# Performance work log

Hardware: AMD Instinct MI355X
Metric: run time of the kernel (lower is better)

Reference implementation:

```python
import jax, jax.numpy as jnp
import numpy as np

B, K, D, H, T, S = 8192, 32, 768, 256, 16, 2  # batch, candidates, d_model, hidden, topics, shots
MAX_SHOT = 8
TEMP = 0.1


def _l2n(x, eps=1e-12):
    return x / jnp.clip(jnp.linalg.norm(x, axis=-1, keepdims=True), eps)


def setup_inputs() -> dict:
    key = jax.random.key(0)
    ks = jax.random.split(key, 20)
    f32 = jnp.float32
    rn = lambda k, shape, s: jax.random.normal(k, shape, f32) * s
    inp = {}
    inp['query_emb'] = jax.random.normal(ks[0], (B, D), f32)
    inp['cand_emb'] = jax.random.normal(ks[1], (B, K, D), f32)
    inp['W_in'] = rn(ks[2], (H, D), 0.03)              # input_proj (bias=False)
    inp['Wq_a'] = rn(ks[3], (H, H), 0.05)              # MHA in-proj q
    inp['Wk_a'] = rn(ks[4], (H, H), 0.05)
    inp['Wv_a'] = rn(ks[5], (H, H), 0.05)
    inp['bq_a'] = jnp.zeros((H,), f32)
    inp['bk_a'] = jnp.zeros((H,), f32)
    inp['bv_a'] = jnp.zeros((H,), f32)
    inp['Wo_a'] = rn(ks[6], (H, H), 0.05)              # MHA out-proj
    inp['bo_a'] = jnp.zeros((H,), f32)
    inp['ln_w'] = jnp.ones((H,), f32)
    inp['ln_b'] = jnp.zeros((H,), f32)
    inp['Wq'] = jnp.eye(H, dtype=f32) + rn(ks[7], (H, H), 0.01)   # query_proj (eye init + noise)
    inp['Wc'] = jnp.eye(H, dtype=f32) + rn(ks[8], (H, H), 0.01)   # cand_proj
    inp['W_ih'] = rn(ks[9], (3 * H, H), 0.05)          # GRUCell ih (r,z,n)
    inp['W_hh'] = rn(ks[10], (3 * H, H), 0.05)
    inp['b_ih'] = jnp.zeros((3 * H,), f32)
    inp['b_hh'] = jnp.zeros((3 * H,), f32)
    inp['step_emb'] = rn(ks[11], (MAX_SHOT, H), 0.02)
    inp['topic_protos'] = rn(ks[12], (T, H), 0.02)
    inp['Wqt'] = rn(ks[13], (T, H), 0.05)              # query_topic_head
    inp['bqt'] = jnp.zeros((T,), f32)
    inp['cover_lambda'] = jnp.array(-2.0, f32)
    return inp


def reference(query_emb, cand_emb, W_in, Wq_a, Wk_a, Wv_a, bq_a, bk_a, bv_a,
              Wo_a, bo_a, ln_w, ln_b, Wq, Wc, W_ih, W_hh, b_ih, b_hh,
              step_emb, topic_protos, Wqt, bqt, cover_lambda):
    Bd = query_emb.shape[0]
    # input projection 768 -> 256
    qr = query_emb @ W_in.T                                # [B,H]
    cr = jnp.einsum('bkd,hd->bkh', cand_emb, W_in)         # [B,K,H]
    # single-head cross-attention (query len 1, eval mode -> no dropout)
    q = qr @ Wq_a.T + bq_a
    k = jnp.einsum('bkh,gh->bkg', cr, Wk_a) + bk_a
    v = jnp.einsum('bkh,gh->bkg', cr, Wv_a) + bv_a
    attn = jax.nn.softmax(jnp.einsum('bh,bkh->bk', q, k) / jnp.sqrt(jnp.float32(H)))
    ctx = jnp.einsum('bk,bkh->bh', attn, v) @ Wo_a.T + bo_a
    # residual + LayerNorm
    x = ctx + qr
    mu = jnp.mean(x, -1, keepdims=True)
    var = jnp.var(x, -1, keepdims=True)
    qe = (x - mu) / jnp.sqrt(var + 1e-5) * ln_w + ln_b
    # pointer projections + L2 normalize
    h = _l2n(qe @ Wq.T)                                    # [B,H]
    cn = _l2n(jnp.einsum('bkh,gh->bkg', cr, Wc))           # [B,K,H]
    topic_probs = jax.nn.softmax(jnp.einsum('bkh,th->bkt', cn, _l2n(topic_protos)))  # [B,K,T]
    need = jax.nn.softmax(h @ Wqt.T + bqt)                 # [B,T]
    lam = jax.nn.softplus(cover_lambda)
    sel = jnp.zeros((Bd, K), bool)
    covered = jnp.zeros((Bd, T), jnp.float32)
    rows = jnp.arange(Bd)
    logits, preds = [], []
    for step in range(S):
        h_step = _l2n(h + step_emb[min(step, MAX_SHOT - 1)])
        scores = jnp.einsum('bh,bkh->bk', h_step, cn) / TEMP
        if step > 0:
            uncov = jnp.clip(1.0 - covered, 0.0, 1.0)
            gain = jnp.einsum('bt,bkt->bk', need * uncov, topic_probs)
            scores = scores + lam * gain
        scores = jnp.where(sel, -100.0, scores)
        logits.append(scores)
        idx = jnp.argmax(scores, axis=-1)                  # labels=None -> greedy feedback
        preds.append(idx)
        sel = sel.at[rows, idx].set(True)
        chosen = cn[rows, idx]                             # [B,H]
        covered = jnp.minimum(covered + topic_probs[rows, idx], 1.0)
        # GRUCell update
        gi = chosen @ W_ih.T + b_ih
        gh = h @ W_hh.T + b_hh
        ir, iz, ig = jnp.split(gi, 3, axis=-1)
        hr, hz, hg = jnp.split(gh, 3, axis=-1)
        r = jax.nn.sigmoid(ir + hr)
        z = jax.nn.sigmoid(iz + hz)
        n = jnp.tanh(ig + r * hg)
        h = _l2n((1.0 - z) * n + z * h)
    return jnp.stack(logits, 1), jnp.stack(preds, 1)       # [B,S,K], [B,S]
```

## Files before the change

kernel.cpp:

```cpp
#include <hip/hip_runtime.h>
#include <math.h>

#define B_ 8192
#define K_ 32
#define D_ 768
#define H_ 256
#define T_ 16
#define S_ 2

typedef unsigned int uint;
typedef unsigned short ushort;
typedef __attribute__((ext_vector_type(8))) short bf16x8;
typedef __attribute__((ext_vector_type(4))) float f32x4;

__device__ __forceinline__ float wsum(float v) {
  v += __shfl_xor(v, 32); v += __shfl_xor(v, 16); v += __shfl_xor(v, 8);
  v += __shfl_xor(v, 4);  v += __shfl_xor(v, 2);  v += __shfl_xor(v, 1);
  return v;
}
__device__ __forceinline__ float wmaxr(float v) {
  v = fmaxf(v, __shfl_xor(v, 32)); v = fmaxf(v, __shfl_xor(v, 16));
  v = fmaxf(v, __shfl_xor(v, 8));  v = fmaxf(v, __shfl_xor(v, 4));
  v = fmaxf(v, __shfl_xor(v, 2));  v = fmaxf(v, __shfl_xor(v, 1));
  return v;
}

__device__ __forceinline__ void split4(const float4 f, uint2& h, uint2& lo) {
  const uint ux = __float_as_uint(f.x), uy = __float_as_uint(f.y);
  const uint uz = __float_as_uint(f.z), uw = __float_as_uint(f.w);
  h.x = (uy & 0xFFFF0000u) | (ux >> 16);
  h.y = (uw & 0xFFFF0000u) | (uz >> 16);
  const float rx = f.x - __uint_as_float(ux & 0xFFFF0000u);
  const float ry = f.y - __uint_as_float(uy & 0xFFFF0000u);
  const float rz = f.z - __uint_as_float(uz & 0xFFFF0000u);
  const float rw = f.w - __uint_as_float(uw & 0xFFFF0000u);
  lo.x = (__float_as_uint(ry) & 0xFFFF0000u) | (__float_as_uint(rx) >> 16);
  lo.y = (__float_as_uint(rw) & 0xFFFF0000u) | (__float_as_uint(rz) >> 16);
}

__device__ __forceinline__ float dot4(const float4 a, const float4 b) {
  float s = a.x * b.x;
  s = fmaf(a.y, b.y, s); s = fmaf(a.z, b.z, s); s = fmaf(a.w, b.w, s);
  return s;
}


__global__ __launch_bounds__(256)
void fold_kernel(const float* __restrict__ Wk_a, const float* __restrict__ Wv_a,
                 const float* __restrict__ Wc,  const float* __restrict__ W_in,
                 float* __restrict__ WkinT, float* __restrict__ Wv_in,
                 ushort* __restrict__ Bh, ushort* __restrict__ Bl)
{
  const int i = blockIdx.x;
  const int m = blockIdx.y;
  const float* Wx = (m == 0) ? Wk_a : ((m == 1) ? Wv_a : Wc);
  const int t = threadIdx.x;
  float a0 = 0.f, a1 = 0.f, a2 = 0.f;
  for (int k = 0; k < H_; k++) {
    const float wv = Wx[i * H_ + k];
    const float* row = W_in + (size_t)k * D_;
    a0 = fmaf(wv, row[t], a0);
    a1 = fmaf(wv, row[t + 256], a1);
    a2 = fmaf(wv, row[t + 512], a2);
  }
  if (m == 0) {
    WkinT[(size_t)t * H_ + i] = a0;
    WkinT[(size_t)(t + 256) * H_ + i] = a1;
    WkinT[(size_t)(t + 512) * H_ + i] = a2;
  } else if (m == 1) {
    float* o = Wv_in + (size_t)i * D_;
    o[t] = a0; o[t + 256] = a1; o[t + 512] = a2;
  } else {
    const float vals[3] = {a0, a1, a2};
#pragma unroll
    for (int j = 0; j < 3; j++) {
      const int k = t + j * 256;
      const float v = vals[j];
      const int idx = (((k >> 5) * 16 + (i >> 4)) * 64 + ((i & 15) | (((k >> 3) & 3) << 4))) * 8 + (k & 7);
      const uint u = __float_as_uint(v);
      Bh[idx] = (ushort)(u >> 16);
      const float rr = v - __uint_as_float(u & 0xFFFF0000u);
      Bl[idx] = (ushort)(__float_as_uint(rr) >> 16);
    }
  }
}

struct TileJob { const float* W; ushort* Bh; ushort* Bl; int NB; int K; int rows; };
struct TileJobs { TileJob j[6]; };

__global__ __launch_bounds__(256)
void tile_all(TileJobs jobs)
{
  const TileJob J = jobs.j[blockIdx.y];
  const int n = blockIdx.x;
  if (n >= J.rows) return;
  const int t = threadIdx.x;
  for (int k = t; k < J.K; k += 256) {
    const float v = J.W[(size_t)n * J.K + k];
    const int idx = (((k >> 5) * J.NB + (n >> 4)) * 64 + ((n & 15) | (((k >> 3) & 3) << 4))) * 8 + (k & 7);
    const uint u = __float_as_uint(v);
    J.Bh[idx] = (ushort)(u >> 16);
    const float rr = v - __uint_as_float(u & 0xFFFF0000u);
    J.Bl[idx] = (ushort)(__float_as_uint(rr) >> 16);
  }
}

__global__ __launch_bounds__(256)
void proto_kernel(const float* __restrict__ tpro, float* __restrict__ pro)
{
  const int w = threadIdx.x >> 6, l = threadIdx.x & 63;
  for (int r = w; r < T_; r += 4) {
    const float4 v = *(const float4*)(tpro + (size_t)r * H_ + l * 4);
    const float n = fmaxf(sqrtf(wsum(v.x * v.x + v.y * v.y + v.z * v.z + v.w * v.w)), 1e-12f);
    float4 o; o.x = v.x / n; o.y = v.y / n; o.z = v.z / n; o.w = v.w / n;
    *(float4*)(pro + (size_t)r * H_ + l * 4) = o;
  }
}

__global__ __launch_bounds__(256)
void fold2_kernel(const float* __restrict__ Wq_a, const float* __restrict__ bq_a,
                  const float* __restrict__ bk_a, const float* __restrict__ Wo_a,
                  const float* __restrict__ bo_a, const float* __restrict__ bv_a,
                  const float* __restrict__ Wq,   const float* __restrict__ ln_w,
                  const float* __restrict__ ln_b, const float* __restrict__ WkinT,
                  const float* __restrict__ Wv_in,
                  float* __restrict__ Bqk, float* __restrict__ bqk,
                  float* __restrict__ Wvo, float* __restrict__ bvo,
                  float* __restrict__ Wqp, float* __restrict__ bqp,
                  float* __restrict__ vqbk, float* __restrict__ qcst)
{
  __shared__ float rd_s[4];
  const int n = blockIdx.x, t = threadIdx.x, w = t >> 6, l = t & 63;
  float s = 0.f;
  for (int hh = 0; hh < H_; hh++)
    s = fmaf(Wq_a[hh * H_ + t], WkinT[(size_t)n * H_ + hh], s);
  Bqk[(size_t)n * H_ + t] = s;
  float p = bq_a[t] * WkinT[(size_t)n * H_ + t];
  p = wsum(p);
  if (l == 0) rd_s[w] = p;
  __syncthreads();
  if (t == 0) bqk[n] = rd_s[0] + rd_s[1] + rd_s[2] + rd_s[3];
  if (n < H_) {
    float a0 = 0.f, a1 = 0.f, a2 = 0.f;
    for (int hh = 0; hh < H_; hh++) {
      const float wo = Wo_a[n * H_ + hh];
      const float* rowv = Wv_in + (size_t)hh * D_;
      a0 = fmaf(wo, rowv[t], a0);
      a1 = fmaf(wo, rowv[t + 256], a1);
      a2 = fmaf(wo, rowv[t + 512], a2);
    }
    Wvo[(size_t)n * D_ + t] = a0;
    Wvo[(size_t)n * D_ + t + 256] = a1;
    Wvo[(size_t)n * D_ + t + 512] = a2;
    float pb = Wo_a[n * H_ + t] * bv_a[t];
    pb = wsum(pb);
    __syncthreads();
    if (l == 0) rd_s[w] = pb;
    __syncthreads();
    if (t == 0) bvo[n] = rd_s[0] + rd_s[1] + rd_s[2] + rd_s[3] + bo_a[n];
    Wqp[n * H_ + t] = Wq[n * H_ + t] * ln_w[t];
    float pq = Wq[n * H_ + t] * ln_b[t];
    pq = wsum(pq);
    __syncthreads();
    if (l == 0) rd_s[w] = pq;
    __syncthreads();
    if (t == 0) bqp[n] = rd_s[0] + rd_s[1] + rd_s[2] + rd_s[3];
  }
  if (n == 0) {
    float sv = 0.f;
    for (int hh = 0; hh < H_; hh++) sv = fmaf(bk_a[hh], Wq_a[hh * H_ + t], sv);
    vqbk[t] = sv;
    float pc = bq_a[t] * bk_a[t];
    pc = wsum(pc);
    __syncthreads();
    if (l == 0) rd_s[w] = pc;
    __syncthreads();
    if (t == 0) qcst[0] = rd_s[0] + rd_s[1] + rd_s[2] + rd_s[3];
  }
}

__global__ __launch_bounds__(256, 3)
void gemm_cn_attn(const float* __restrict__ A, const ushort* __restrict__ Bh,
                  const ushort* __restrict__ Bl, const float* __restrict__ qkv,
                  const float* __restrict__ qr, const float* __restrict__ vqbk,
                  const float* __restrict__ qcst, float* __restrict__ C,
                  float* __restrict__ wce)
{
  __shared__ __align__(16) ushort AhS[2][2048], AlS[2][2048];
  __shared__ __align__(16) float4 qkv_s[384];
  __shared__ float sc_s[64], at_s[64], qbk_s[2];
  __shared__ float rsq[64][4];
  const int t = threadIdx.x, l = t & 63, w = t >> 6;
  const int r = t >> 2, kc = t & 3;
  const int tb = t >> 7;
  const float* Ag = A + ((size_t)blockIdx.x * 64 + r) * 768 + kc * 8;
  const int aslot = ((r >> 4) * 64 + ((r & 15) | (kc << 4))) * 8;
  const ushort* Bhb = Bh + ((w * 4) * 64 + l) * 8;
  const ushort* Blb = Bl + ((w * 4) * 64 + l) * 8;

  for (int i = t; i < 384; i += 256)
    qkv_s[i] = ((const float4*)qkv)[(size_t)blockIdx.x * 384 + i];
  if (w < 2) {
    const float4 q4 = ((const float4*)qr)[((size_t)blockIdx.x * 2 + w) * 64 + l];
    const float4 v4 = ((const float4*)vqbk)[l];
    float p = wsum(dot4(q4, v4));
    if (l == 0) qbk_s[w] = p + qcst[0];
  }

  f32x4 acc[4][4];
#pragma unroll
  for (int i = 0; i < 4; i++)
#pragma unroll
    for (int j = 0; j < 4; j++) acc[i][j] = (f32x4)0.f;

  float sc = 0.f;
  float4 f0 = *(const float4*)(Ag);
  float4 f1 = *(const float4*)(Ag + 4);
  __syncthreads();
  sc += dot4(f0, qkv_s[tb * 192 + kc * 2]) + dot4(f1, qkv_s[tb * 192 + kc * 2 + 1]);
  {
    uint2 ha, la, hb, lb;
    split4(f0, ha, la); split4(f1, hb, lb);
    *(uint4*)&AhS[0][aslot] = make_uint4(ha.x, ha.y, hb.x, hb.y);
    *(uint4*)&AlS[0][aslot] = make_uint4(la.x, la.y, lb.x, lb.y);
  }
  f0 = *(const float4*)(Ag + 32);
  f1 = *(const float4*)(Ag + 36);
  __syncthreads();

#pragma unroll 2
  for (int ks = 0; ks < 24; ks++) {
    const int cur = ks & 1;
    uint4 bhv[4], blv[4];
#pragma unroll
    for (int ni = 0; ni < 4; ni++) {
      bhv[ni] = *(const uint4*)(Bhb + ks * 8192 + ni * 512);
      blv[ni] = *(const uint4*)(Blb + ks * 8192 + ni * 512);
    }
    if (ks < 23) {
      sc += dot4(f0, qkv_s[tb * 192 + (ks + 1) * 8 + kc * 2]) +
            dot4(f1, qkv_s[tb * 192 + (ks + 1) * 8 + kc * 2 + 1]);
      uint2 ha, la, hb, lb;
      split4(f0, ha, la); split4(f1, hb, lb);
      *(uint4*)&AhS[cur ^ 1][aslot] = make_uint4(ha.x, ha.y, hb.x, hb.y);
      *(uint4*)&AlS[cur ^ 1][aslot] = make_uint4(la.x, la.y, lb.x, lb.y);
      if (ks < 22) {
        f0 = *(const float4*)(Ag + (ks + 2) * 32);
        f1 = *(const float4*)(Ag + (ks + 2) * 32 + 4);
      }
    }
#pragma unroll
    for (int mi = 0; mi < 4; mi++) {
      const bf16x8 ah = *(const bf16x8*)&AhS[cur][(mi * 64 + l) * 8];
      const bf16x8 al = *(const bf16x8*)&AlS[cur][(mi * 64 + l) * 8];
#pragma unroll
      for (int ni = 0; ni < 4; ni++) {
        const bf16x8 bhf = *(const bf16x8*)&bhv[ni];
        const bf16x8 blf = *(const bf16x8*)&blv[ni];
        acc[mi][ni] = __builtin_amdgcn_mfma_f32_16x16x32_bf16(ah, bhf, acc[mi][ni], 0, 0, 0);
        acc[mi][ni] = __builtin_amdgcn_mfma_f32_16x16x32_bf16(al, bhf, acc[mi][ni], 0, 0, 0);
        acc[mi][ni] = __builtin_amdgcn_mfma_f32_16x16x32_bf16(ah, blf, acc[mi][ni], 0, 0, 0);
      }
    }
    __syncthreads();
  }

  sc += __shfl_xor(sc, 1);
  sc += __shfl_xor(sc, 2);
  if ((t & 3) == 0) sc_s[r] = sc;
  __syncthreads();
  if (w < 2) {
    float s = (l < 32) ? (sc_s[w * 32 + l] + qbk_s[w]) * (1.f / 16.f) : -1e30f;
    const float m = wmaxr(s);
    const float e = (l < 32) ? expf(s - m) : 0.f;
    const float su = wsum(e);
    if (l < 32) at_s[w * 32 + l] = e / su;
  }
  __syncthreads();
#pragma unroll
  for (int p = 0; p < 2; p++) {
    const int slot = t + p * 256;
    if (slot < 384) {
      const int tb2 = slot >= 192;
      const int idx = slot - tb2 * 192;
      const float4* cb = (const float4*)A + ((size_t)blockIdx.x * 64 + tb2 * 32) * 192 + idx;
      float4 a = make_float4(0.f, 0.f, 0.f, 0.f);
#pragma unroll 4
      for (int c = 0; c < 32; c++) {
        const float av = at_s[tb2 * 32 + c];
        const float4 f = cb[c * 192];
        a.x = fmaf(av, f.x, a.x); a.y = fmaf(av, f.y, a.y);
        a.z = fmaf(av, f.z, a.z); a.w = fmaf(av, f.w, a.w);
      }
      ((float4*)wce)[((size_t)blockIdx.x * 2 + tb2) * 192 + idx] = a;
    }
  }

#pragma unroll
  for (int mi = 0; mi < 4; mi++)
#pragma unroll
    for (int rg = 0; rg < 4; rg++) {
      float p = 0.f;
#pragma unroll
      for (int ni = 0; ni < 4; ni++) { const float v = acc[mi][ni][rg]; p = fmaf(v, v, p); }
      p += __shfl_xor(p, 1); p += __shfl_xor(p, 2); p += __shfl_xor(p, 4); p += __shfl_xor(p, 8);
      if ((l & 15) == 0) rsq[mi * 16 + (l >> 4) * 4 + rg][w] = p;
    }
  __syncthreads();
  const size_t row0 = (size_t)blockIdx.x * 64;
#pragma unroll
  for (int mi = 0; mi < 4; mi++)
#pragma unroll
    for (int rg = 0; rg < 4; rg++) {
      const int rl = mi * 16 + (l >> 4) * 4 + rg;
      const float ssum = rsq[rl][0] + rsq[rl][1] + rsq[rl][2] + rsq[rl][3];
      const float inv = 1.f / fmaxf(sqrtf(ssum), 1e-12f);
#pragma unroll
      for (int ni = 0; ni < 4; ni++)
        C[(row0 + rl) * H_ + w * 64 + ni * 16 + (l & 15)] = acc[mi][ni][rg] * inv;
    }
}

__global__ __launch_bounds__(256, 3)
void gemm_ctx_ln(const float* __restrict__ A, const ushort* __restrict__ Bh,
                 const ushort* __restrict__ Bl, const float* __restrict__ bvo,
                 const float* __restrict__ qr, float* __restrict__ xhat)
{
  __shared__ __align__(16) ushort AhS[2][2048], AlS[2][2048];
  __shared__ float red[64][4][2];
  const int t = threadIdx.x, l = t & 63, w = t >> 6;
  const int r = t >> 2, kc = t & 3;
  const float* Ag = A + ((size_t)blockIdx.x * 64 + r) * 768 + kc * 8;
  const int aslot = ((r >> 4) * 64 + ((r & 15) | (kc << 4))) * 8;
  const ushort* Bhb = Bh + ((w * 4) * 64 + l) * 8;
  const ushort* Blb = Bl + ((w * 4) * 64 + l) * 8;

  f32x4 acc[4][4];
#pragma unroll
  for (int i = 0; i < 4; i++)
#pragma unroll
    for (int j = 0; j < 4; j++) acc[i][j] = (f32x4)0.f;

  float4 f0 = *(const float4*)(Ag);
  float4 f1 = *(const float4*)(Ag + 4);
  {
    uint2 ha, la, hb, lb;
    split4(f0, ha, la); split4(f1, hb, lb);
    *(uint4*)&AhS[0][aslot] = make_uint4(ha.x, ha.y, hb.x, hb.y);
    *(uint4*)&AlS[0][aslot] = make_uint4(la.x, la.y, lb.x, lb.y);
  }
  f0 = *(const float4*)(Ag + 32);
  f1 = *(const float4*)(Ag + 36);
  __syncthreads();

#pragma unroll 2
  for (int ks = 0; ks < 24; ks++) {
    const int cur = ks & 1;
    uint4 bhv[4], blv[4];
#pragma unroll
    for (int ni = 0; ni < 4; ni++) {
      bhv[ni] = *(const uint4*)(Bhb + ks * 8192 + ni * 512);
      blv[ni] = *(const uint4*)(Blb + ks * 8192 + ni * 512);
    }
    if (ks < 23) {
      uint2 ha, la, hb, lb;
      split4(f0, ha, la); split4(f1, hb, lb);
      *(uint4*)&AhS[cur ^ 1][aslot] = make_uint4(ha.x, ha.y, hb.x, hb.y);
      *(uint4*)&AlS[cur ^ 1][aslot] = make_uint4(la.x, la.y, lb.x, lb.y);
      if (ks < 22) {
        f0 = *(const float4*)(Ag + (ks + 2) * 32);
        f1 = *(const float4*)(Ag + (ks + 2) * 32 + 4);
      }
    }
#pragma unroll
    for (int mi = 0; mi < 4; mi++) {
      const bf16x8 ah = *(const bf16x8*)&AhS[cur][(mi * 64 + l) * 8];
      const bf16x8 al = *(const bf16x8*)&AlS[cur][(mi * 64 + l) * 8];
#pragma unroll
      for (int ni = 0; ni < 4; ni++) {
        const bf16x8 bhf = *(const bf16x8*)&bhv[ni];
        const bf16x8 blf = *(const bf16x8*)&blv[ni];
        acc[mi][ni] = __builtin_amdgcn_mfma_f32_16x16x32_bf16(ah, bhf, acc[mi][ni], 0, 0, 0);
        acc[mi][ni] = __builtin_amdgcn_mfma_f32_16x16x32_bf16(al, bhf, acc[mi][ni], 0, 0, 0);
        acc[mi][ni] = __builtin_amdgcn_mfma_f32_16x16x32_bf16(ah, blf, acc[mi][ni], 0, 0, 0);
      }
    }
    __syncthreads();
  }

  const size_t row0 = (size_t)blockIdx.x * 64;
#pragma unroll
  for (int mi = 0; mi < 4; mi++)
#pragma unroll
    for (int rg = 0; rg < 4; rg++) {
      const int rl = mi * 16 + (l >> 4) * 4 + rg;
      float sx = 0.f, sxx = 0.f;
#pragma unroll
      for (int ni = 0; ni < 4; ni++) {
        const int col = w * 64 + ni * 16 + (l & 15);
        const float x = acc[mi][ni][rg] + bvo[col] + qr[(row0 + rl) * H_ + col];
        acc[mi][ni][rg] = x;
        sx += x; sxx = fmaf(x, x, sxx);
      }
      sx += __shfl_xor(sx, 1); sx += __shfl_xor(sx, 2); sx += __shfl_xor(sx, 4); sx += __shfl_xor(sx, 8);
      sxx += __shfl_xor(sxx, 1); sxx += __shfl_xor(sxx, 2); sxx += __shfl_xor(sxx, 4); sxx += __shfl_xor(sxx, 8);
      if ((l & 15) == 0) { red[rl][w][0] = sx; red[rl][w][1] = sxx; }
    }
  __syncthreads();
#pragma unroll
  for (int mi = 0; mi < 4; mi++)
#pragma unroll
    for (int rg = 0; rg < 4; rg++) {
      const int rl = mi * 16 + (l >> 4) * 4 + rg;
      const float SX = red[rl][0][0] + red[rl][1][0] + red[rl][2][0] + red[rl][3][0];
      const float SXX = red[rl][0][1] + red[rl][1][1] + red[rl][2][1] + red[rl][3][1];
      const float mu = SX * (1.f / H_);
      const float var = SXX * (1.f / H_) - mu * mu;
      const float isd = 1.f / sqrtf(var + 1e-5f);
#pragma unroll
      for (int ni = 0; ni < 4; ni++)
        xhat[(row0 + rl) * H_ + w * 64 + ni * 16 + (l & 15)] = (acc[mi][ni][rg] - mu) * isd;
    }
}

template<int NKS, int NB, bool BIAS>
__global__ __launch_bounds__(256)
void gemm_bf(const float* __restrict__ A, const ushort* __restrict__ Bh,
             const ushort* __restrict__ Bl, const float* __restrict__ bias,
             float* __restrict__ C)
{
  __shared__ __align__(16) ushort AhS[2][4096], AlS[2][4096];
  const int t = threadIdx.x, l = t & 63, w = t >> 6;
  const int wr = w >> 1, wc = w & 1;
  const int Kd = NKS * 32, N = NB * 16;
  const int r = t >> 1, kc0 = (t & 1) * 2;
  const float* Ag = A + ((size_t)blockIdx.x * 128 + r) * Kd + kc0 * 8;
  const int aslot0 = ((r >> 4) * 64 + ((r & 15) | (kc0 << 4))) * 8;
  const int aslot1 = aslot0 + 128;
  const int nb0 = blockIdx.y * 4 + wc * 2;
  const ushort* Bhb = Bh + (nb0 * 64 + l) * 8;
  const ushort* Blb = Bl + (nb0 * 64 + l) * 8;

  f32x4 acc[4][2];
#pragma unroll
  for (int i = 0; i < 4; i++)
#pragma unroll
    for (int j = 0; j < 2; j++) acc[i][j] = (f32x4)0.f;

  float4 f0 = *(const float4*)(Ag);
  float4 f1 = *(const float4*)(Ag + 4);
  float4 f2 = *(const float4*)(Ag + 8);
  float4 f3 = *(const float4*)(Ag + 12);
  {
    uint2 ha, la, hb, lb;
    split4(f0, ha, la); split4(f1, hb, lb);
    *(uint4*)&AhS[0][aslot0] = make_uint4(ha.x, ha.y, hb.x, hb.y);
    *(uint4*)&AlS[0][aslot0] = make_uint4(la.x, la.y, lb.x, lb.y);
    split4(f2, ha, la); split4(f3, hb, lb);
    *(uint4*)&AhS[0][aslot1] = make_uint4(ha.x, ha.y, hb.x, hb.y);
    *(uint4*)&AlS[0][aslot1] = make_uint4(la.x, la.y, lb.x, lb.y);
  }
  f0 = *(const float4*)(Ag + 32); f1 = *(const float4*)(Ag + 36);
  f2 = *(const float4*)(Ag + 40); f3 = *(const float4*)(Ag + 44);
  __syncthreads();

#pragma unroll 2
  for (int ks = 0; ks < NKS; ks++) {
    const int cur = ks & 1;
    if (ks < NKS - 1) {
      uint2 ha, la, hb, lb;
      split4(f0, ha, la); split4(f1, hb, lb);
      *(uint4*)&AhS[cur ^ 1][aslot0] = make_uint4(ha.x, ha.y, hb.x, hb.y);
      *(uint4*)&AlS[cur ^ 1][aslot0] = make_uint4(la.x, la.y, lb.x, lb.y);
      split4(f2, ha, la); split4(f3, hb, lb);
      *(uint4*)&AhS[cur ^ 1][aslot1] = make_uint4(ha.x, ha.y, hb.x, hb.y);
      *(uint4*)&AlS[cur ^ 1][aslot1] = make_uint4(la.x, la.y, lb.x, lb.y);
      if (ks < NKS - 2) {
        f0 = *(const float4*)(Ag + (ks + 2) * 32);
        f1 = *(const float4*)(Ag + (ks + 2) * 32 + 4);
        f2 = *(const float4*)(Ag + (ks + 2) * 32 + 8);
        f3 = *(const float4*)(Ag + (ks + 2) * 32 + 12);
      }
    }
#pragma unroll
    for (int mi = 0; mi < 4; mi++) {
      const bf16x8 ah = *(const bf16x8*)&AhS[cur][((wr * 4 + mi) * 64 + l) * 8];
      const bf16x8 al = *(const bf16x8*)&AlS[cur][((wr * 4 + mi) * 64 + l) * 8];
#pragma unroll
      for (int ni = 0; ni < 2; ni++) {
        const bf16x8 bhf = *(const bf16x8*)(Bhb + ks * (NB * 512) + ni * 512);
        const bf16x8 blf = *(const bf16x8*)(Blb + ks * (NB * 512) + ni * 512);
        acc[mi][ni] = __builtin_amdgcn_mfma_f32_16x16x32_bf16(ah, bhf, acc[mi][ni], 0, 0, 0);
        acc[mi][ni] = __builtin_amdgcn_mfma_f32_16x16x32_bf16(al, bhf, acc[mi][ni], 0, 0, 0);
        acc[mi][ni] = __builtin_amdgcn_mfma_f32_16x16x32_bf16(ah, blf, acc[mi][ni], 0, 0, 0);
      }
    }
    __syncthreads();
  }

  const size_t row0 = (size_t)blockIdx.x * 128 + wr * 64;
  const int col0 = blockIdx.y * 64 + wc * 32;
#pragma unroll
  for (int mi = 0; mi < 4; mi++)
#pragma unroll
    for (int ni = 0; ni < 2; ni++) {
      const int col = col0 + ni * 16 + (l & 15);
      const float bb = BIAS ? bias[col] : 0.f;
#pragma unroll
      for (int rg = 0; rg < 4; rg++) {
        const size_t row = row0 + mi * 16 + (l >> 4) * 4 + rg;
        C[row * N + col] = acc[mi][ni][rg] + bb;
      }
    }
}

__global__ __launch_bounds__(256)
void h_post(const float* __restrict__ hraw, const float* __restrict__ Wqt,
            const float* __restrict__ bqt, float* __restrict__ h, float* __restrict__ need)
{
  __shared__ float wq_s[T_ * H_];
  for (int i = threadIdx.x; i < T_ * H_; i += 256) wq_s[i] = Wqt[i];
  const int w = threadIdx.x >> 6, l = threadIdx.x & 63;
  const size_t r = (size_t)blockIdx.x * 4 + w;
  const float4 v = *(const float4*)(hraw + r * H_ + l * 4);
  const float n = fmaxf(sqrtf(wsum(v.x * v.x + v.y * v.y + v.z * v.z + v.w * v.w)), 1e-12f);
  float4 hn; hn.x = v.x / n; hn.y = v.y / n; hn.z = v.z / n; hn.w = v.w / n;
  *(float4*)(h + r * H_ + l * 4) = hn;
  __syncthreads();
  float mine = 0.f;
  for (int tt = 0; tt < T_; tt++) {
    const float4 p4 = *(const float4*)(wq_s + tt * H_ + l * 4);
    float p = hn.x * p4.x + hn.y * p4.y + hn.z * p4.z + hn.w * p4.w;
    p = wsum(p);
    if (l == tt) mine = p + bqt[l];
  }
  float s = (l < T_) ? mine : -1e30f;
  const float m = wmaxr(s);
  const float e = (l < T_) ? expf(s - m) : 0.f;
  const float su = wsum(e);
  if (l < T_) need[r * T_ + l] = e / su;
}

__global__ __launch_bounds__(256)
void score0_kernel(const float* __restrict__ h, const float* __restrict__ se,
                   const float* __restrict__ cn, const float* __restrict__ pro,
                   float* __restrict__ covered, float* __restrict__ chosen,
                   float* __restrict__ logits, float* __restrict__ preds)
{
  __shared__ __align__(16) float hs_s[H_];
  __shared__ __align__(16) float cr_s[H_];
  __shared__ float part_s[T_ * 16];
  __shared__ float sc_s[K_];
  __shared__ float rd_s[4];
  __shared__ int idx_s;
  const int b = blockIdx.x, t = threadIdx.x;
  const int w = t >> 6, l = t & 63;

  const float hv = h[(size_t)b * H_ + t] + se[t];
  const float ss = wsum(hv * hv);
  if (l == 0) rd_s[w] = ss;
  __syncthreads();
  const float n = fmaxf(sqrtf(rd_s[0] + rd_s[1] + rd_s[2] + rd_s[3]), 1e-12f);
  hs_s[t] = hv / n;
  __syncthreads();

  const float4 hf = *(const float4*)(hs_s + l * 4);
#pragma unroll
  for (int cc = 0; cc < 8; cc++) {
    const int c = w * 8 + cc;
    const float4 cv = *(const float4*)(cn + ((size_t)b * K_ + c) * H_ + l * 4);
    float p = wsum(dot4(cv, hf));
    if (l == 0) sc_s[c] = p * 10.f;
  }
  __syncthreads();
  if (w == 0) {
    float s = (l < K_) ? sc_s[l] : -1e30f;
    int bi = (l < K_) ? l : K_;
#pragma unroll
    for (int o = 32; o; o >>= 1) {
      const float s2 = __shfl_xor(s, o);
      const int i2 = __shfl_xor(bi, o);
      if (s2 > s || (s2 == s && i2 < bi)) { s = s2; bi = i2; }
    }
    if (l == 0) idx_s = bi;
  }
  __syncthreads();
  const int idx = idx_s;
  if (t < K_) logits[(size_t)b * (S_ * K_) + t] = sc_s[t];
  if (t == 0) preds[(size_t)b * S_] = (float)idx;

  const float crv = cn[((size_t)b * K_ + idx) * H_ + t];
  cr_s[t] = crv;
  chosen[(size_t)b * H_ + t] = crv;
  __syncthreads();
  {
    const int tt = t & 15, ch = t >> 4;
    float p = 0.f;
#pragma unroll
    for (int j = 0; j < 16; j++)
      p = fmaf(cr_s[ch * 16 + j], pro[tt * H_ + ch * 16 + j], p);
    part_s[tt * 16 + ch] = p;
  }
  __syncthreads();
  if (t < 16) {
    float d = 0.f;
#pragma unroll
    for (int ch = 0; ch < 16; ch++) d += part_s[t * 16 + ch];
    float mx = d;
    mx = fmaxf(mx, __shfl_xor(mx, 1)); mx = fmaxf(mx, __shfl_xor(mx, 2));
    mx = fmaxf(mx, __shfl_xor(mx, 4)); mx = fmaxf(mx, __shfl_xor(mx, 8));
    const float e = expf(d - mx);
    float su = e;
    su += __shfl_xor(su, 1); su += __shfl_xor(su, 2);
    su += __shfl_xor(su, 4); su += __shfl_xor(su, 8);
    covered[(size_t)b * T_ + t] = fminf(e / su, 1.f);
  }
}

__global__ __launch_bounds__(256)
void score1_kernel(const float* __restrict__ gi, const float* __restrict__ gh,
                   const float* __restrict__ h,  const float* __restrict__ se,
                   const float* __restrict__ cn, const float* __restrict__ pro,
                   const float* __restrict__ need, const float* __restrict__ clam,
                   const float* __restrict__ covered,
                   float* __restrict__ logits, float* __restrict__ preds)
{
  __shared__ __align__(16) float cn_s[K_ * 260];
  __shared__ __align__(16) float pro_s[T_ * 260];
  __shared__ __align__(16) float hs_s[H_];
  __shared__ float gd_s[K_ * T_];
  __shared__ float gain_s[K_];
  __shared__ float nu_s[T_], sc_s[K_], rd_s[4], rd2_s[4];
  const int b = blockIdx.x, t = threadIdx.x;
  const int w = t >> 6, l = t & 63;

  const size_t o = (size_t)b * (3 * H_);
  const float ir = gi[o + t], iz = gi[o + 256 + t], ig = gi[o + 512 + t];
  const float hr = gh[o + t], hz = gh[o + 256 + t], hg = gh[o + 512 + t];
  const float hv = h[(size_t)b * H_ + t];
  const float rr = 1.f / (1.f + expf(-(ir + hr)));
  const float zz = 1.f / (1.f + expf(-(iz + hz)));
  const float nn = tanhf(ig + rr * hg);
  const float x = (1.f - zz) * nn + zz * hv;
  const float ss = wsum(x * x);
  if (l == 0) rd_s[w] = ss;

  {
    const float4* cng = (const float4*)(cn + (size_t)b * K_ * H_);
    float4* cns4 = (float4*)cn_s;
    for (int i = t; i < 2048; i += 256) cns4[(i >> 6) * 65 + (i & 63)] = cng[i];
    const float4* prg = (const float4*)pro;
    float4* prs4 = (float4*)pro_s;
    for (int i = t; i < 1024; i += 256) prs4[(i >> 6) * 65 + (i & 63)] = prg[i];
  }
  if (t < T_)
    nu_s[t] = need[(size_t)b * T_ + t] * fminf(fmaxf(1.f - covered[(size_t)b * T_ + t], 0.f), 1.f);
  __syncthreads();
  const float n1 = fmaxf(sqrtf(rd_s[0] + rd_s[1] + rd_s[2] + rd_s[3]), 1e-12f);
  const float y = x / n1 + se[H_ + t];
  const float ss2 = wsum(y * y);
  if (l == 0) rd2_s[w] = ss2;
  __syncthreads();
  const float n2 = fmaxf(sqrtf(rd2_s[0] + rd2_s[1] + rd2_s[2] + rd2_s[3]), 1e-12f);
  hs_s[t] = y / n2;
  __syncthreads();

  const float4* cn_s4 = (const float4*)cn_s;
  const float4* pro_s4 = (const float4*)pro_s;
  const float4 hf = *(const float4*)(hs_s + l * 4);
#pragma unroll
  for (int cc = 0; cc < 8; cc++) {
    const int c = w * 8 + cc;
    const float4 cv = cn_s4[c * 65 + l];
    float p = wsum(dot4(cv, hf));
    if (l == 0) sc_s[c] = p * 10.f;
  }
#pragma unroll
  for (int pr = 0; pr < 2; pr++) {
    const int idx2 = t + pr * 256;
    const int c = idx2 >> 4, tt = idx2 & 15;
    float d = 0.f;
#pragma unroll 8
    for (int j = 0; j < 64; j++)
      d += dot4(cn_s4[c * 65 + j], pro_s4[tt * 65 + j]);
    gd_s[idx2] = d;
  }
  __syncthreads();
  if (t < K_) {
    float mx = -1e30f;
#pragma unroll
    for (int tt = 0; tt < T_; tt++) mx = fmaxf(mx, gd_s[t * T_ + tt]);
    float su = 0.f, ga = 0.f;
#pragma unroll
    for (int tt = 0; tt < T_; tt++) {
      const float e = expf(gd_s[t * T_ + tt] - mx);
      su += e; ga = fmaf(nu_s[tt], e, ga);
    }
    gain_s[t] = ga / su;
  }
  const int i0 = (int)preds[(size_t)b * S_];
  __syncthreads();
  if (w == 0) {
    const float lam = log1pf(expf(clam[0]));
    float s = (l < K_) ? sc_s[l] + lam * gain_s[l] : -1e30f;
    if (l < K_ && l == i0) s = -100.f;
    if (l < K_) logits[(size_t)b * (S_ * K_) + K_ + l] = s;
    int bi = (l < K_) ? l : K_;
    float sm = s;
#pragma unroll
    for (int o2 = 32; o2; o2 >>= 1) {
      const float s2 = __shfl_xor(sm, o2);
      const int i2 = __shfl_xor(bi, o2);
      if (s2 > sm || (s2 == sm && i2 < bi)) { sm = s2; bi = i2; }
    }
    if (l == 0) preds[(size_t)b * S_ + 1] = (float)bi;
  }
}

extern "C" void kernel_launch(void* const* d_in, const int* in_sizes, int n_in,
                              void* d_out, int out_size, void* d_ws, size_t ws_size,
                              hipStream_t stream)
{
  const float* query_emb = (const float*)d_in[0];
  const float* cand_emb  = (const float*)d_in[1];
  const float* W_in = (const float*)d_in[2];
  const float* Wq_a = (const float*)d_in[3];
  const float* Wk_a = (const float*)d_in[4];
  const float* Wv_a = (const float*)d_in[5];
  const float* bq_a = (const float*)d_in[6];
  const float* bk_a = (const float*)d_in[7];
  const float* bv_a = (const float*)d_in[8];
  const float* Wo_a = (const float*)d_in[9];
  const float* bo_a = (const float*)d_in[10];
  const float* ln_w = (const float*)d_in[11];
  const float* ln_b = (const float*)d_in[12];
  const float* Wq   = (const float*)d_in[13];
  const float* Wc   = (const float*)d_in[14];
  const float* W_ih = (const float*)d_in[15];
  const float* W_hh = (const float*)d_in[16];
  const float* b_ih = (const float*)d_in[17];
  const float* b_hh = (const float*)d_in[18];
  const float* step_emb = (const float*)d_in[19];
  const float* tpro = (const float*)d_in[20];
  const float* Wqt  = (const float*)d_in[21];
  const float* bqt  = (const float*)d_in[22];
  const float* clam = (const float*)d_in[23];

  float* ws = (float*)d_ws;
  size_t o = 0;
  float* WkinT = ws + o; o += (size_t)D_ * H_;
  float* Wv_in = ws + o; o += (size_t)H_ * D_;
  ushort* BhW  = (ushort*)(ws + o); o += 98304;
  ushort* BlW  = (ushort*)(ws + o); o += 98304;
  float* pro   = ws + o; o += (size_t)T_ * H_;
  float* Bqk   = ws + o; o += (size_t)D_ * H_;
  float* bqk   = ws + o; o += 1024;
  float* Wvo   = ws + o; o += (size_t)H_ * D_;
  float* bvo   = ws + o; o += 256;
  float* Wqp   = ws + o; o += (size_t)H_ * H_;
  float* bqp   = ws + o; o += 256;
  float* vqbk  = ws + o; o += 256;
  float* qcst  = ws + o; o += 4;
  ushort* WintH = (ushort*)(ws + o); o += 98304;
  ushort* WintL = (ushort*)(ws + o); o += 98304;
  ushort* BqktH = (ushort*)(ws + o); o += 98304;
  ushort* BqktL = (ushort*)(ws + o); o += 98304;
  ushort* WvotH = (ushort*)(ws + o); o += 98304;
  ushort* WvotL = (ushort*)(ws + o); o += 98304;
  ushort* WqptH = (ushort*)(ws + o); o += 32768;
  ushort* WqptL = (ushort*)(ws + o); o += 32768;
  ushort* WihtH = (ushort*)(ws + o); o += 98304;
  ushort* WihtL = (ushort*)(ws + o); o += 98304;
  ushort* WhhtH = (ushort*)(ws + o); o += 98304;
  ushort* WhhtL = (ushort*)(ws + o); o += 98304;
  float* qr    = ws + o; o += (size_t)B_ * H_;
  float* qkv   = ws + o; o += (size_t)B_ * D_;
  float* wce   = ws + o; o += (size_t)B_ * D_;
  float* ctxb  = ws + o; o += (size_t)B_ * H_;
  float* xhat  = ws + o; o += (size_t)B_ * H_;
  float* h     = ws + o; o += (size_t)B_ * H_;
  float* need  = ws + o; o += (size_t)B_ * T_;
  float* cn    = ws + o; o += (size_t)B_ * K_ * H_;
  float* cov   = ws + o; o += (size_t)B_ * T_;
  float* chosen= ws + o; o += (size_t)B_ * H_;

  float* out_logits = (float*)d_out;
  float* out_preds  = (float*)d_out + (size_t)B_ * S_ * K_;

  fold_kernel<<<dim3(H_, 3), 256, 0, stream>>>(Wk_a, Wv_a, Wc, W_in, WkinT, Wv_in, BhW, BlW);
  proto_kernel<<<1, 256, 0, stream>>>(tpro, pro);
  fold2_kernel<<<D_, 256, 0, stream>>>(Wq_a, bq_a, bk_a, Wo_a, bo_a, bv_a, Wq, ln_w, ln_b,
                                       WkinT, Wv_in, Bqk, bqk, Wvo, bvo, Wqp, bqp, vqbk, qcst);
  TileJobs jobs;
  jobs.j[0] = {W_in, WintH, WintL, 16, 768, 256};
  jobs.j[1] = {Bqk,  BqktH, BqktL, 48, 256, 768};
  jobs.j[2] = {Wvo,  WvotH, WvotL, 16, 768, 256};
  jobs.j[3] = {Wqp,  WqptH, WqptL, 16, 256, 256};
  jobs.j[4] = {W_ih, WihtH, WihtL, 48, 256, 768};
  jobs.j[5] = {W_hh, WhhtH, WhhtL, 48, 256, 768};
  tile_all<<<dim3(768, 6), 256, 0, stream>>>(jobs);

  gemm_bf<24, 16, false><<<dim3(B_ / 128, 4), 256, 0, stream>>>(query_emb, WintH, WintL, nullptr, qr);
  gemm_bf<8, 48, true><<<dim3(B_ / 128, 12), 256, 0, stream>>>(qr, BqktH, BqktL, bqk, qkv);

  gemm_cn_attn<<<(B_ * K_) / 64, 256, 0, stream>>>(cand_emb, BhW, BlW, qkv, qr, vqbk, qcst, cn, wce);

  gemm_ctx_ln<<<B_ / 64, 256, 0, stream>>>(wce, WvotH, WvotL, bvo, qr, xhat);
  gemm_bf<8, 16, true><<<dim3(B_ / 128, 4), 256, 0, stream>>>(xhat, WqptH, WqptL, bqp, ctxb);
  h_post<<<B_ / 4, 256, 0, stream>>>(ctxb, Wqt, bqt, h, need);

  score0_kernel<<<B_, 256, 0, stream>>>(h, step_emb, cn, pro, cov, chosen, out_logits, out_preds);
  gemm_bf<8, 48, true><<<dim3(B_ / 128, 12), 256, 0, stream>>>(chosen, WihtH, WihtL, b_ih, qkv);
  gemm_bf<8, 48, true><<<dim3(B_ / 128, 12), 256, 0, stream>>>(h, WhhtH, WhhtL, b_hh, wce);
  score1_kernel<<<B_, 256, 0, stream>>>(qkv, wce, h, step_emb, cn, pro, need, clam, cov,
                                        out_logits, out_preds);
}
```

Baseline: 883.5 us.

## Load A fragments directly from global into MFMA registers, drop LDS staging

The three GEMM kernels no longer stage the A operand through double-buffered shared memory with per-step barriers. Each lane now reads its MFMA fragment straight from global memory, splits it into bf16 hi/lo in registers, and feeds the MFMAs. gemm_ctx_ln is also retiled to 32 rows per block with twice as many blocks. This removes LDS traffic and __syncthreads, but all four waves now read the same A rows redundantly and the software prefetch overlap is gone, which leaves more exposed global load latency.

```diff
diff --git a/kernel.cpp b/kernel.cpp
--- a/kernel.cpp
+++ b/kernel.cpp
@@ -36,6 +36,17 @@
   const float rw = f.w - __uint_as_float(uw & 0xFFFF0000u);
   lo.x = (__float_as_uint(ry) & 0xFFFF0000u) | (__float_as_uint(rx) >> 16);
   lo.y = (__float_as_uint(rw) & 0xFFFF0000u) | (__float_as_uint(rz) >> 16);
+}
+
+__device__ __forceinline__ bf16x8 mk8(const uint2 a, const uint2 b) {
+  union { uint4 u; bf16x8 v; } x;
+  x.u = make_uint4(a.x, a.y, b.x, b.y);
+  return x.v;
+}
+__device__ __forceinline__ bf16x8 u2b(const uint4 u) {
+  union { uint4 u; bf16x8 v; } x;
+  x.u = u;
+  return x.v;
 }
 
 __device__ __forceinline__ float dot4(const float4 a, const float4 b) {
@@ -186,17 +197,10 @@
                   const float* __restrict__ qcst, float* __restrict__ C,
                   float* __restrict__ wce)
 {
-  __shared__ __align__(16) ushort AhS[2][2048], AlS[2][2048];
   __shared__ __align__(16) float4 qkv_s[384];
   __shared__ float sc_s[64], at_s[64], qbk_s[2];
   __shared__ float rsq[64][4];
   const int t = threadIdx.x, l = t & 63, w = t >> 6;
-  const int r = t >> 2, kc = t & 3;
-  const int tb = t >> 7;
-  const float* Ag = A + ((size_t)blockIdx.x * 64 + r) * 768 + kc * 8;
-  const int aslot = ((r >> 4) * 64 + ((r & 15) | (kc << 4))) * 8;
-  const ushort* Bhb = Bh + ((w * 4) * 64 + l) * 8;
-  const ushort* Blb = Bl + ((w * 4) * 64 + l) * 8;
 
   for (int i = t; i < 384; i += 256)
     qkv_s[i] = ((const float4*)qkv)[(size_t)blockIdx.x * 384 + i];
@@ -207,67 +211,49 @@
     if (l == 0) qbk_s[w] = p + qcst[0];
   }
 
+  const float* Arow = A + ((size_t)blockIdx.x * 64 + (l & 15)) * 768 + (l >> 4) * 8;
+  const ushort* Bhb = Bh + ((w * 4) * 64 + l) * 8;
+  const ushort* Blb = Bl + ((w * 4) * 64 + l) * 8;
+  const int qbase = (w >> 1) * 192 + (l >> 4) * 2;
+
   f32x4 acc[4][4];
 #pragma unroll
   for (int i = 0; i < 4; i++)
 #pragma unroll
     for (int j = 0; j < 4; j++) acc[i][j] = (f32x4)0.f;
-
   float sc = 0.f;
-  float4 f0 = *(const float4*)(Ag);
-  float4 f1 = *(const float4*)(Ag + 4);
-  __syncthreads();
-  sc += dot4(f0, qkv_s[tb * 192 + kc * 2]) + dot4(f1, qkv_s[tb * 192 + kc * 2 + 1]);
-  {
-    uint2 ha, la, hb, lb;
-    split4(f0, ha, la); split4(f1, hb, lb);
-    *(uint4*)&AhS[0][aslot] = make_uint4(ha.x, ha.y, hb.x, hb.y);
-    *(uint4*)&AlS[0][aslot] = make_uint4(la.x, la.y, lb.x, lb.y);
-  }
-  f0 = *(const float4*)(Ag + 32);
-  f1 = *(const float4*)(Ag + 36);
-  __syncthreads();
-
-#pragma unroll 2
+  __syncthreads();
+
   for (int ks = 0; ks < 24; ks++) {
-    const int cur = ks & 1;
     uint4 bhv[4], blv[4];
 #pragma unroll
     for (int ni = 0; ni < 4; ni++) {
       bhv[ni] = *(const uint4*)(Bhb + ks * 8192 + ni * 512);
       blv[ni] = *(const uint4*)(Blb + ks * 8192 + ni * 512);
     }
-    if (ks < 23) {
-      sc += dot4(f0, qkv_s[tb * 192 + (ks + 1) * 8 + kc * 2]) +
-            dot4(f1, qkv_s[tb * 192 + (ks + 1) * 8 + kc * 2 + 1]);
+    const float4 q0 = qkv_s[qbase + ks * 8];
+    const float4 q1 = qkv_s[qbase + ks * 8 + 1];
+#pragma unroll
+    for (int mi = 0; mi < 4; mi++) {
+      const float4 f0 = *(const float4*)(Arow + (size_t)mi * 16 * 768 + ks * 32);
+      const float4 f1 = *(const float4*)(Arow + (size_t)mi * 16 * 768 + ks * 32 + 4);
+      if (mi == w) sc += dot4(f0, q0) + dot4(f1, q1);
       uint2 ha, la, hb, lb;
       split4(f0, ha, la); split4(f1, hb, lb);
-      *(uint4*)&AhS[cur ^ 1][aslot] = make_uint4(ha.x, ha.y, hb.x, hb.y);
-      *(uint4*)&AlS[cur ^ 1][aslot] = make_uint4(la.x, la.y, lb.x, lb.y);
-      if (ks < 22) {
-        f0 = *(const float4*)(Ag + (ks + 2) * 32);
-        f1 = *(const float4*)(Ag + (ks + 2) * 32 + 4);
+      const bf16x8 ah = mk8(ha, hb);
+      const bf16x8 al = mk8(la, lb);
+#pragma unroll
+      for (int ni = 0; ni < 4; ni++) {
+        acc[mi][ni] = __builtin_amdgcn_mfma_f32_16x16x32_bf16(ah, u2b(bhv[ni]), acc[mi][ni], 0, 0, 0);
+        acc[mi][ni] = __builtin_amdgcn_mfma_f32_16x16x32_bf16(al, u2b(bhv[ni]), acc[mi][ni], 0, 0, 0);
+        acc[mi][ni] = __builtin_amdgcn_mfma_f32_16x16x32_bf16(ah, u2b(blv[ni]), acc[mi][ni], 0, 0, 0);
       }
     }
-#pragma unroll
-    for (int mi = 0; mi < 4; mi++) {
-      const bf16x8 ah = *(const bf16x8*)&AhS[cur][(mi * 64 + l) * 8];
-      const bf16x8 al = *(const bf16x8*)&AlS[cur][(mi * 64 + l) * 8];
-#pragma unroll
-      for (int ni = 0; ni < 4; ni++) {
-        const bf16x8 bhf = *(const bf16x8*)&bhv[ni];
-        const bf16x8 blf = *(const bf16x8*)&blv[ni];
-        acc[mi][ni] = __builtin_amdgcn_mfma_f32_16x16x32_bf16(ah, bhf, acc[mi][ni], 0, 0, 0);
-        acc[mi][ni] = __builtin_amdgcn_mfma_f32_16x16x32_bf16(al, bhf, acc[mi][ni], 0, 0, 0);
-        acc[mi][ni] = __builtin_amdgcn_mfma_f32_16x16x32_bf16(ah, blf, acc[mi][ni], 0, 0, 0);
-      }
-    }
-    __syncthreads();
-  }
-
-  sc += __shfl_xor(sc, 1);
-  sc += __shfl_xor(sc, 2);
-  if ((t & 3) == 0) sc_s[r] = sc;
+  }
+
+  sc += __shfl_xor(sc, 16);
+  sc += __shfl_xor(sc, 32);
+  if (l < 16) sc_s[w * 16 + l] = sc;
   __syncthreads();
   if (w < 2) {
     float s = (l < 32) ? (sc_s[w * 32 + l] + qbk_s[w]) * (1.f / 16.f) : -1e30f;
@@ -321,76 +307,50 @@
     }
 }
 
-__global__ __launch_bounds__(256, 3)
+__global__ __launch_bounds__(256)
 void gemm_ctx_ln(const float* __restrict__ A, const ushort* __restrict__ Bh,
                  const ushort* __restrict__ Bl, const float* __restrict__ bvo,
                  const float* __restrict__ qr, float* __restrict__ xhat)
 {
-  __shared__ __align__(16) ushort AhS[2][2048], AlS[2][2048];
-  __shared__ float red[64][4][2];
+  __shared__ float red[32][4][2];
   const int t = threadIdx.x, l = t & 63, w = t >> 6;
-  const int r = t >> 2, kc = t & 3;
-  const float* Ag = A + ((size_t)blockIdx.x * 64 + r) * 768 + kc * 8;
-  const int aslot = ((r >> 4) * 64 + ((r & 15) | (kc << 4))) * 8;
+  const float* Arow = A + ((size_t)blockIdx.x * 32 + (l & 15)) * 768 + (l >> 4) * 8;
   const ushort* Bhb = Bh + ((w * 4) * 64 + l) * 8;
   const ushort* Blb = Bl + ((w * 4) * 64 + l) * 8;
 
-  f32x4 acc[4][4];
-#pragma unroll
-  for (int i = 0; i < 4; i++)
+  f32x4 acc[2][4];
+#pragma unroll
+  for (int i = 0; i < 2; i++)
 #pragma unroll
     for (int j = 0; j < 4; j++) acc[i][j] = (f32x4)0.f;
 
-  float4 f0 = *(const float4*)(Ag);
-  float4 f1 = *(const float4*)(Ag + 4);
-  {
-    uint2 ha, la, hb, lb;
-    split4(f0, ha, la); split4(f1, hb, lb);
-    *(uint4*)&AhS[0][aslot] = make_uint4(ha.x, ha.y, hb.x, hb.y);
-    *(uint4*)&AlS[0][aslot] = make_uint4(la.x, la.y, lb.x, lb.y);
-  }
-  f0 = *(const float4*)(Ag + 32);
-  f1 = *(const float4*)(Ag + 36);
-  __syncthreads();
-
-#pragma unroll 2
   for (int ks = 0; ks < 24; ks++) {
-    const int cur = ks & 1;
     uint4 bhv[4], blv[4];
 #pragma unroll
     for (int ni = 0; ni < 4; ni++) {
       bhv[ni] = *(const uint4*)(Bhb + ks * 8192 + ni * 512);
       blv[ni] = *(const uint4*)(Blb + ks * 8192 + ni * 512);
     }
-    if (ks < 23) {
+#pragma unroll
+    for (int mi = 0; mi < 2; mi++) {
+      const float4 f0 = *(const float4*)(Arow + (size_t)mi * 16 * 768 + ks * 32);
+      const float4 f1 = *(const float4*)(Arow + (size_t)mi * 16 * 768 + ks * 32 + 4);
       uint2 ha, la, hb, lb;
       split4(f0, ha, la); split4(f1, hb, lb);
-      *(uint4*)&AhS[cur ^ 1][aslot] = make_uint4(ha.x, ha.y, hb.x, hb.y);
-      *(uint4*)&AlS[cur ^ 1][aslot] = make_uint4(la.x, la.y, lb.x, lb.y);
-      if (ks < 22) {
-        f0 = *(const float4*)(Ag + (ks + 2) * 32);
-        f1 = *(const float4*)(Ag + (ks + 2) * 32 + 4);
+      const bf16x8 ah = mk8(ha, hb);
+      const bf16x8 al = mk8(la, lb);
+#pragma unroll
+      for (int ni = 0; ni < 4; ni++) {
+        acc[mi][ni] = __builtin_amdgcn_mfma_f32_16x16x32_bf16(ah, u2b(bhv[ni]), acc[mi][ni], 0, 0, 0);
+        acc[mi][ni] = __builtin_amdgcn_mfma_f32_16x16x32_bf16(al, u2b(bhv[ni]), acc[mi][ni], 0, 0, 0);
+        acc[mi][ni] = __builtin_amdgcn_mfma_f32_16x16x32_bf16(ah, u2b(blv[ni]), acc[mi][ni], 0, 0, 0);
       }
     }
-#pragma unroll
-    for (int mi = 0; mi < 4; mi++) {
-      const bf16x8 ah = *(const bf16x8*)&AhS[cur][(mi * 64 + l) * 8];
-      const bf16x8 al = *(const bf16x8*)&AlS[cur][(mi * 64 + l) * 8];
-#pragma unroll
-      for (int ni = 0; ni < 4; ni++) {
-        const bf16x8 bhf = *(const bf16x8*)&bhv[ni];
-        const bf16x8 blf = *(const bf16x8*)&blv[ni];
-        acc[mi][ni] = __builtin_amdgcn_mfma_f32_16x16x32_bf16(ah, bhf, acc[mi][ni], 0, 0, 0);
-        acc[mi][ni] = __builtin_amdgcn_mfma_f32_16x16x32_bf16(al, bhf, acc[mi][ni], 0, 0, 0);
-        acc[mi][ni] = __builtin_amdgcn_mfma_f32_16x16x32_bf16(ah, blf, acc[mi][ni], 0, 0, 0);
-      }
-    }
-    __syncthreads();
-  }
-
-  const size_t row0 = (size_t)blockIdx.x * 64;
-#pragma unroll
-  for (int mi = 0; mi < 4; mi++)
+  }
+
+  const size_t row0 = (size_t)blockIdx.x * 32;
+#pragma unroll
+  for (int mi = 0; mi < 2; mi++)
 #pragma unroll
     for (int rg = 0; rg < 4; rg++) {
       const int rl = mi * 16 + (l >> 4) * 4 + rg;
@@ -408,7 +368,7 @@
     }
   __syncthreads();
 #pragma unroll
-  for (int mi = 0; mi < 4; mi++)
+  for (int mi = 0; mi < 2; mi++)
 #pragma unroll
     for (int rg = 0; rg < 4; rg++) {
       const int rl = mi * 16 + (l >> 4) * 4 + rg;
@@ -429,14 +389,10 @@
              const ushort* __restrict__ Bl, const float* __restrict__ bias,
              float* __restrict__ C)
 {
-  __shared__ __align__(16) ushort AhS[2][4096], AlS[2][4096];
   const int t = threadIdx.x, l = t & 63, w = t >> 6;
   const int wr = w >> 1, wc = w & 1;
   const int Kd = NKS * 32, N = NB * 16;
-  const int r = t >> 1, kc0 = (t & 1) * 2;
-  const float* Ag = A + ((size_t)blockIdx.x * 128 + r) * Kd + kc0 * 8;
-  const int aslot0 = ((r >> 4) * 64 + ((r & 15) | (kc0 << 4))) * 8;
-  const int aslot1 = aslot0 + 128;
+  const float* Arow = A + ((size_t)blockIdx.x * 128 + wr * 64 + (l & 15)) * Kd + (l >> 4) * 8;
   const int nb0 = blockIdx.y * 4 + wc * 2;
   const ushort* Bhb = Bh + (nb0 * 64 + l) * 8;
   const ushort* Blb = Bl + (nb0 * 64 + l) * 8;
@@ -447,55 +403,28 @@
 #pragma unroll
     for (int j = 0; j < 2; j++) acc[i][j] = (f32x4)0.f;
 
-  float4 f0 = *(const float4*)(Ag);
-  float4 f1 = *(const float4*)(Ag + 4);
-  float4 f2 = *(const float4*)(Ag + 8);
-  float4 f3 = *(const float4*)(Ag + 12);
-  {
-    uint2 ha, la, hb, lb;
-    split4(f0, ha, la); split4(f1, hb, lb);
-    *(uint4*)&AhS[0][aslot0] = make_uint4(ha.x, ha.y, hb.x, hb.y);
-    *(uint4*)&AlS[0][aslot0] = make_uint4(la.x, la.y, lb.x, lb.y);
-    split4(f2, ha, la); split4(f3, hb, lb);
-    *(uint4*)&AhS[0][aslot1] = make_uint4(ha.x, ha.y, hb.x, hb.y);
-    *(uint4*)&AlS[0][aslot1] = make_uint4(la.x, la.y, lb.x, lb.y);
-  }
-  f0 = *(const float4*)(Ag + 32); f1 = *(const float4*)(Ag + 36);
-  f2 = *(const float4*)(Ag + 40); f3 = *(const float4*)(Ag + 44);
-  __syncthreads();
-
-#pragma unroll 2
   for (int ks = 0; ks < NKS; ks++) {
-    const int cur = ks & 1;
-    if (ks < NKS - 1) {
+    uint4 bhv[2], blv[2];
+#pragma unroll
+    for (int ni = 0; ni < 2; ni++) {
+      bhv[ni] = *(const uint4*)(Bhb + ks * (NB * 512) + ni * 512);
+      blv[ni] = *(const uint4*)(Blb + ks * (NB * 512) + ni * 512);
+    }
+#pragma unroll
+    for (int mi = 0; mi < 4; mi++) {
+      const float4 f0 = *(const float4*)(Arow + (size_t)mi * 16 * Kd + ks * 32);
+      const float4 f1 = *(const float4*)(Arow + (size_t)mi * 16 * Kd + ks * 32 + 4);
       uint2 ha, la, hb, lb;
       split4(f0, ha, la); split4(f1, hb, lb);
-      *(uint4*)&AhS[cur ^ 1][aslot0] = make_uint4(ha.x, ha.y, hb.x, hb.y);
-      *(uint4*)&AlS[cur ^ 1][aslot0] = make_uint4(la.x, la.y, lb.x, lb.y);
-      split4(f2, ha, la); split4(f3, hb, lb);
-      *(uint4*)&AhS[cur ^ 1][aslot1] = make_uint4(ha.x, ha.y, hb.x, hb.y);
-      *(uint4*)&AlS[cur ^ 1][aslot1] = make_uint4(la.x, la.y, lb.x, lb.y);
-      if (ks < NKS - 2) {
-        f0 = *(const float4*)(Ag + (ks + 2) * 32);
-        f1 = *(const float4*)(Ag + (ks + 2) * 32 + 4);
-        f2 = *(const float4*)(Ag + (ks + 2) * 32 + 8);
-        f3 = *(const float4*)(Ag + (ks + 2) * 32 + 12);
+      const bf16x8 ah = mk8(ha, hb);
+      const bf16x8 al = mk8(la, lb);
+#pragma unroll
+      for (int ni = 0; ni < 2; ni++) {
+        acc[mi][ni] = __builtin_amdgcn_mfma_f32_16x16x32_bf16(ah, u2b(bhv[ni]), acc[mi][ni], 0, 0, 0);
+        acc[mi][ni] = __builtin_amdgcn_mfma_f32_16x16x32_bf16(al, u2b(bhv[ni]), acc[mi][ni], 0, 0, 0);
+        acc[mi][ni] = __builtin_amdgcn_mfma_f32_16x16x32_bf16(ah, u2b(blv[ni]), acc[mi][ni], 0, 0, 0);
       }
     }
-#pragma unroll
-    for (int mi = 0; mi < 4; mi++) {
-      const bf16x8 ah = *(const bf16x8*)&AhS[cur][((wr * 4 + mi) * 64 + l) * 8];
-      const bf16x8 al = *(const bf16x8*)&AlS[cur][((wr * 4 + mi) * 64 + l) * 8];
-#pragma unroll
-      for (int ni = 0; ni < 2; ni++) {
-        const bf16x8 bhf = *(const bf16x8*)(Bhb + ks * (NB * 512) + ni * 512);
-        const bf16x8 blf = *(const bf16x8*)(Blb + ks * (NB * 512) + ni * 512);
-        acc[mi][ni] = __builtin_amdgcn_mfma_f32_16x16x32_bf16(ah, bhf, acc[mi][ni], 0, 0, 0);
-        acc[mi][ni] = __builtin_amdgcn_mfma_f32_16x16x32_bf16(al, bhf, acc[mi][ni], 0, 0, 0);
-        acc[mi][ni] = __builtin_amdgcn_mfma_f32_16x16x32_bf16(ah, blf, acc[mi][ni], 0, 0, 0);
-      }
-    }
-    __syncthreads();
   }
 
   const size_t row0 = (size_t)blockIdx.x * 128 + wr * 64;
@@ -805,7 +734,7 @@
 
   gemm_cn_attn<<<(B_ * K_) / 64, 256, 0, stream>>>(cand_emb, BhW, BlW, qkv, qr, vqbk, qcst, cn, wce);
 
-  gemm_ctx_ln<<<B_ / 64, 256, 0, stream>>>(wce, WvotH, WvotL, bvo, qr, xhat);
+  gemm_ctx_ln<<<B_ / 32, 256, 0, stream>>>(wce, WvotH, WvotL, bvo, qr, xhat);
   gemm_bf<8, 16, true><<<dim3(B_ / 128, 4), 256, 0, stream>>>(xhat, WqptH, WqptL, bqp, ctxb);
   h_post<<<B_ / 4, 256, 0, stream>>>(ctxb, Wqt, bqt, h, need);
 
```

After: 1.218 ms. 37.8% more time.
